# Optimization experiments

Measured on AMD Instinct MI355X. Metric: run time of the kernel, lower is better.

Reference implementation:

```python
import jax, jax.numpy as jnp
import numpy as np

B, T, E = 2, 4096, 768
H = 12
WIN = 256  # one-sided window w; band width = 2w+1


def setup_inputs() -> dict:
    key = jax.random.key(0)
    k1, k2, k3, k4 = jax.random.split(key, 4)
    scale = 1.0 / np.sqrt(E)
    return {
        "x": jax.random.normal(k1, (B, T, E), dtype=jnp.float32),
        "Wq": jax.random.normal(k2, (E, E), dtype=jnp.float32) * scale,
        "Wk": jax.random.normal(k3, (E, E), dtype=jnp.float32) * scale,
        "Wv": jax.random.normal(k4, (E, E), dtype=jnp.float32) * scale,
    }


def reference(x, Wq, Wk, Wv):
    b, t, e = x.shape
    h, w = H, WIN
    s = e // h
    Wb = 2 * w + 1          # band width
    nc = t // w             # number of query chunks of size w

    # projections (nn.Linear, bias=False): y = x @ W^T
    q = (x @ Wq.T).reshape(b, t, h, s) * (1.0 / np.sqrt(s))
    k = (x @ Wk.T).reshape(b, t, h, s)
    v = (x @ Wv.T).reshape(b, t, h, s)

    # overlapping key/value chunks: chunk c covers absolute keys [c*w - w, c*w + 2w)
    pad = [(0, 0), (w, w), (0, 0), (0, 0)]
    kp = jnp.pad(k, pad).reshape(b, nc + 2, w, h, s)
    k3 = jnp.concatenate([kp[:, :-2], kp[:, 1:-1], kp[:, 2:]], axis=2)  # [b,nc,3w,h,s]
    vp = jnp.pad(v, pad).reshape(b, nc + 2, w, h, s)
    v3 = jnp.concatenate([vp[:, :-2], vp[:, 1:-1], vp[:, 2:]], axis=2)  # [b,nc,3w,h,s]

    qc = q.reshape(b, nc, w, h, s)
    scores = jnp.einsum('bcxhd,bcyhd->bhcxy', qc, k3)  # [b,h,nc,w,3w]

    # extract the banded diagonals: band j <-> key index p + j in the 3w window
    idx = jnp.arange(w)[:, None] + jnp.arange(Wb)[None, :]  # [w, 2w+1], values in [0,3w)
    band = jnp.take_along_axis(scores, idx[None, None, None], axis=-1)  # [b,h,nc,w,2w+1]
    band = band.reshape(b, h, t, Wb).transpose(0, 2, 1, 3)  # [b,t,h,2w+1]

    # mask_invalid_locations: key absolute pos = i + j - w must lie in [0, t)
    key_pos = jnp.arange(t)[:, None] + jnp.arange(Wb)[None, :] - w
    invalid = (key_pos < 0) | (key_pos >= t)
    band = jnp.where(invalid[None, :, None, :], -jnp.inf, band)

    probs = jax.nn.softmax(band.astype(jnp.float32), axis=-1).astype(x.dtype)

    # sliding_chunks_matmul_pv: scatter band probs back to the 3w window layout
    pc = probs.transpose(0, 2, 1, 3).reshape(b, h, nc, w, Wb)
    pc_pad = jnp.pad(pc, [(0, 0)] * 4 + [(w - 1, w - 1)])  # last axis len 4w-1
    # full[p, m] = band[p, m - p] for m-p in [0, 2w], else 0
    idx2 = (jnp.arange(3 * w)[None, :] - jnp.arange(w)[:, None]) + (w - 1)  # [w, 3w]
    pfull = jnp.take_along_axis(pc_pad, idx2[None, None, None], axis=-1)  # [b,h,nc,w,3w]

    out = jnp.einsum('bhcpm,bcmhd->bcphd', pfull, v3).reshape(b, t, e)
    return out
```

## Files before the change

kernel.cpp:

```cpp
#include <hip/hip_runtime.h>

#define B_ 2
#define T_ 4096
#define E_ 768
#define H_ 12
#define S_ 64
#define WIN_ 256

typedef unsigned short u16;
typedef unsigned int u32;
typedef __attribute__((ext_vector_type(8))) short bf16x8;
typedef __attribute__((ext_vector_type(4))) short bf16x4;
typedef __attribute__((ext_vector_type(4))) float f32x4;

__device__ __forceinline__ u16 f2bf(float f) {
  u32 u = __float_as_uint(f);
  u += ((u >> 16) & 1u) + 0x7fffu;
  return (u16)(u >> 16);
}

__device__ __forceinline__ void async_copy16(const u16* g, u16* l) {
  __builtin_amdgcn_global_load_lds(
      (const __attribute__((address_space(1))) void*)g,
      (__attribute__((address_space(3))) void*)l, 16, 0, 0);
}

__global__ void cvt_all(const float* __restrict__ x, const float* __restrict__ wq,
                        const float* __restrict__ wk, const float* __restrict__ wv,
                        u16* __restrict__ xb, u16* __restrict__ wb) {
  const int n4x = B_ * T_ * E_ / 4;
  const int n4w = E_ * E_ / 4;
  int i = blockIdx.x * 256 + threadIdx.x;
  const float* src;
  u16* dst;
  int j;
  if (i < n4x) {
    src = x; dst = xb; j = i;
  } else {
    int t = i - n4x;
    int z = t / n4w;
    if (z >= 3) return;
    j = t - z * n4w;
    src = (z == 0) ? wq : ((z == 1) ? wk : wv);
    dst = wb + (size_t)z * E_ * E_;
  }
  float4 v = ((const float4*)src)[j];
  ushort4 o;
  o.x = f2bf(v.x); o.y = f2bf(v.y); o.z = f2bf(v.z); o.w = f2bf(v.w);
  ((ushort4*)dst)[j] = o;
}

__global__ __launch_bounds__(256)
void gemm_qkv(const u16* __restrict__ xb, const u16* __restrict__ wb,
              u16* __restrict__ qkv) {
  const int M = B_ * T_;
  __shared__ u16 As[3][128][32];
  __shared__ u16 Bs[3][128][32];
  int tid = threadIdx.x;
  int lane = tid & 63, wave = tid >> 6;
  int wr = wave >> 1, wc = wave & 1;
  int q8 = lane >> 4, nl = lane & 15;
  int bm = blockIdx.x * 128, bn = blockIdx.y * 128;
  int z = blockIdx.z;
  const u16* A = xb;
  const u16* Bmat = wb + (size_t)z * E_ * E_;
  u16* C = qkv + (size_t)z * M * E_;
  float scale = (z == 0) ? (0.125f * 1.44269504088896f) : 1.0f;

  int r0 = tid >> 2, c0 = tid & 3;
  int cs = c0 ^ (r0 & 3);
  const u16* ga0 = A + (size_t)(bm + r0) * E_ + cs * 8;
  const u16* ga1 = A + (size_t)(bm + r0 + 64) * E_ + cs * 8;
  const u16* gb0 = Bmat + (size_t)(bn + r0) * E_ + cs * 8;
  const u16* gb1 = Bmat + (size_t)(bn + r0 + 64) * E_ + cs * 8;
  int l0 = tid * 8;
  int l1 = tid * 8 + 2048;

  int swz8 = (q8 ^ (nl & 3)) * 8;

  const int NK = E_ / 32;
#pragma unroll
  for (int p = 0; p < 2; ++p) {
    int koff = p * 32;
    async_copy16(ga0 + koff, &As[p][0][0] + l0);
    async_copy16(ga1 + koff, &As[p][0][0] + l1);
    async_copy16(gb0 + koff, &Bs[p][0][0] + l0);
    async_copy16(gb1 + koff, &Bs[p][0][0] + l1);
  }

  f32x4 acc[4][4] = {};

#define KSTEP(KI, BUF, PBUF)                                                   \
  {                                                                            \
    asm volatile("s_waitcnt vmcnt(4) lgkmcnt(0)" ::: "memory");                \
    __builtin_amdgcn_s_barrier();                                              \
    __builtin_amdgcn_sched_barrier(0);                                         \
    int kp = ((KI) + 2 < NK) ? (KI) + 2 : NK - 1;                              \
    int koff = kp * 32;                                                        \
    async_copy16(ga0 + koff, &As[PBUF][0][0] + l0);                            \
    async_copy16(ga1 + koff, &As[PBUF][0][0] + l1);                            \
    async_copy16(gb0 + koff, &Bs[PBUF][0][0] + l0);                            \
    async_copy16(gb1 + koff, &Bs[PBUF][0][0] + l1);                            \
    bf16x8 af[4], bfr[4];                                                      \
    _Pragma("unroll")                                                          \
    for (int i = 0; i < 4; ++i)                                                \
      af[i] = *(const bf16x8*)&As[BUF][wr * 64 + i * 16 + nl][swz8];           \
    _Pragma("unroll")                                                          \
    for (int i = 0; i < 4; ++i)                                                \
      bfr[i] = *(const bf16x8*)&Bs[BUF][wc * 64 + i * 16 + nl][swz8];          \
    __builtin_amdgcn_s_setprio(1);                                             \
    _Pragma("unroll")                                                          \
    for (int i = 0; i < 4; ++i)                                                \
      _Pragma("unroll")                                                        \
      for (int j2 = 0; j2 < 4; ++j2)                                           \
        acc[i][j2] = __builtin_amdgcn_mfma_f32_16x16x32_bf16(af[i], bfr[j2],   \
                                                             acc[i][j2], 0, 0, 0); \
    __builtin_amdgcn_s_setprio(0);                                             \
  }

  for (int kb = 0; kb < NK; kb += 3) {
    KSTEP(kb + 0, 0, 2)
    KSTEP(kb + 1, 1, 0)
    KSTEP(kb + 2, 2, 1)
  }
#undef KSTEP

#pragma unroll
  for (int i = 0; i < 4; ++i)
#pragma unroll
    for (int j2 = 0; j2 < 4; ++j2)
#pragma unroll
      for (int r = 0; r < 4; ++r) {
        int row = bm + wr * 64 + i * 16 + q8 * 4 + r;
        int col = bn + wc * 64 + j2 * 16 + nl;
        C[(size_t)row * E_ + col] = f2bf(acc[i][j2][r] * scale);
      }
}

__global__ void transpose_v(const u16* __restrict__ v, u16* __restrict__ vT) {
  __shared__ u16 lt[64][66];
  int t = threadIdx.x;
  int t0 = blockIdx.x * 64;
  int e0 = blockIdx.y * 64;
  int b = blockIdx.z;
#pragma unroll
  for (int i = 0; i < 2; ++i) {
    int u = t + i * 256;
    int tok = u >> 3, cg = u & 7;
    bf16x8 val = *(const bf16x8*)(v + (size_t)(b * T_ + t0 + tok) * E_ + e0 + cg * 8);
#pragma unroll
    for (int j = 0; j < 8; ++j) lt[tok][cg * 8 + j] = (u16)val[j];
  }
  __syncthreads();
#pragma unroll
  for (int i = 0; i < 2; ++i) {
    int u = t + i * 256;
    int d = u >> 3, ck = u & 7;
    bf16x8 o;
#pragma unroll
    for (int j = 0; j < 8; ++j) o[j] = (short)lt[ck * 8 + j][d];
    *(bf16x8*)(vT + (size_t)(b * E_ + e0 + d) * T_ + t0 + ck * 8) = o;
  }
}

__global__ __launch_bounds__(256)
void attn_kernel(const u16* __restrict__ qkv, const u16* __restrict__ vT,
                 float* __restrict__ out) {
  const int Mtot = B_ * T_;
  const u16* qb = qkv;
  const u16* kb = qkv + (size_t)Mtot * E_;

  __shared__ u16 Pl[4][2][16][36];

  int tid = threadIdx.x;
  int lane = tid & 63, wave = tid >> 6;
  int q8 = lane >> 4, nl = lane & 15;
  int qs = blockIdx.x * 128;
  int bh = blockIdx.y;
  int b = bh / H_, h = bh % H_;
  int qw = qs + wave * 32;
  size_t ho = (size_t)h * S_;

  bf16x8 aq[2][2];
#pragma unroll
  for (int mt = 0; mt < 2; ++mt) {
    const u16* qrow = qb + (size_t)(b * T_ + qw + mt * 16 + nl) * E_ + ho;
    aq[mt][0] = *(const bf16x8*)(qrow + q8 * 8);
    aq[mt][1] = *(const bf16x8*)(qrow + 32 + q8 * 8);
  }

  f32x4 O[2][4] = {};
  f32x4 lacc[2] = {};

  int klo = qw - WIN_; if (klo < 0) klo = 0;
  int khi = qw + 32 + WIN_; if (khi > T_) khi = T_;

  const u16* kbase = kb + (size_t)b * T_ * E_ + ho;
  const u16* vbase = vT + (size_t)b * E_ * T_ + ho * T_;

  bf16x8 bk[2][2];
#pragma unroll
  for (int nt = 0; nt < 2; ++nt) {
    const u16* krow = kbase + (size_t)(klo + nt * 16 + nl) * E_;
    bk[nt][0] = *(const bf16x8*)(krow + q8 * 8);
    bk[nt][1] = *(const bf16x8*)(krow + 32 + q8 * 8);
  }

  for (int kt = klo; kt < khi; kt += 32) {
    bf16x8 bv[4];
#pragma unroll
    for (int dt = 0; dt < 4; ++dt)
      bv[dt] = *(const bf16x8*)(vbase + (size_t)(dt * 16 + nl) * T_ + kt + q8 * 8);

    int ktn = (kt + 32 < khi) ? kt + 32 : kt;
    bf16x8 nbk[2][2];
#pragma unroll
    for (int nt = 0; nt < 2; ++nt) {
      const u16* krow = kbase + (size_t)(ktn + nt * 16 + nl) * E_;
      nbk[nt][0] = *(const bf16x8*)(krow + q8 * 8);
      nbk[nt][1] = *(const bf16x8*)(krow + 32 + q8 * 8);
    }

    f32x4 sc[2][2] = {};
#pragma unroll
    for (int nt = 0; nt < 2; ++nt)
#pragma unroll
      for (int mt = 0; mt < 2; ++mt) {
        sc[mt][nt] = __builtin_amdgcn_mfma_f32_16x16x32_bf16(aq[mt][0], bk[nt][0], sc[mt][nt], 0, 0, 0);
        sc[mt][nt] = __builtin_amdgcn_mfma_f32_16x16x32_bf16(aq[mt][1], bk[nt][1], sc[mt][nt], 0, 0, 0);
      }

    if (kt < qw - 225 || kt > qw + 225) {
#pragma unroll
      for (int mt = 0; mt < 2; ++mt)
#pragma unroll
        for (int nt = 0; nt < 2; ++nt)
#pragma unroll
          for (int r = 0; r < 4; ++r) {
            int qa = qw + mt * 16 + q8 * 4 + r;
            int ka = kt + nt * 16 + nl;
            int d = ka - qa;
            sc[mt][nt][r] = (d < -WIN_ || d > WIN_) ? -1e30f : sc[mt][nt][r];
          }
    }

#pragma unroll
    for (int mt = 0; mt < 2; ++mt)
#pragma unroll
      for (int r = 0; r < 4; ++r) {
        float p0 = exp2f(sc[mt][0][r]);
        float p1 = exp2f(sc[mt][1][r]);
        sc[mt][0][r] = p0; sc[mt][1][r] = p1;
        lacc[mt][r] += p0 + p1;
      }

#pragma unroll
    for (int mt = 0; mt < 2; ++mt)
#pragma unroll
      for (int r = 0; r < 4; ++r) {
        Pl[wave][mt][q8 * 4 + r][nl] = f2bf(sc[mt][0][r]);
        Pl[wave][mt][q8 * 4 + r][16 + nl] = f2bf(sc[mt][1][r]);
      }

    bf16x8 ap[2];
#pragma unroll
    for (int mt = 0; mt < 2; ++mt) {
      bf16x4 lo = *(const bf16x4*)&Pl[wave][mt][nl][q8 * 8];
      bf16x4 hi = *(const bf16x4*)&Pl[wave][mt][nl][q8 * 8 + 4];
      bf16x8 a;
      a[0] = lo[0]; a[1] = lo[1]; a[2] = lo[2]; a[3] = lo[3];
      a[4] = hi[0]; a[5] = hi[1]; a[6] = hi[2]; a[7] = hi[3];
      ap[mt] = a;
    }

#pragma unroll
    for (int dt = 0; dt < 4; ++dt)
#pragma unroll
      for (int mt = 0; mt < 2; ++mt)
        O[mt][dt] = __builtin_amdgcn_mfma_f32_16x16x32_bf16(ap[mt], bv[dt], O[mt][dt], 0, 0, 0);

#pragma unroll
    for (int nt = 0; nt < 2; ++nt) {
      bk[nt][0] = nbk[nt][0];
      bk[nt][1] = nbk[nt][1];
    }
  }

#pragma unroll
  for (int mt = 0; mt < 2; ++mt)
#pragma unroll
    for (int r = 0; r < 4; ++r) {
      float l = lacc[mt][r];
      l += __shfl_xor(l, 1); l += __shfl_xor(l, 2);
      l += __shfl_xor(l, 4); l += __shfl_xor(l, 8);
      float inv = 1.0f / l;
      int qa = qw + mt * 16 + q8 * 4 + r;
      float* op = out + (size_t)(b * T_ + qa) * E_ + ho;
#pragma unroll
      for (int dt = 0; dt < 4; ++dt)
        op[dt * 16 + nl] = O[mt][dt][r] * inv;
    }
}

extern "C" void kernel_launch(void* const* d_in, const int* in_sizes, int n_in,
                              void* d_out, int out_size, void* d_ws, size_t ws_size,
                              hipStream_t stream) {
  const float* x  = (const float*)d_in[0];
  const float* Wq = (const float*)d_in[1];
  const float* Wk = (const float*)d_in[2];
  const float* Wv = (const float*)d_in[3];
  float* out = (float*)d_out;

  const size_t M = (size_t)B_ * T_;
  u16* xb  = (u16*)d_ws;
  u16* wb  = xb + M * E_;
  u16* qkv = wb + 3 * (size_t)E_ * E_;
  u16* vT  = xb;

  const int n4x = B_ * T_ * E_ / 4;
  const int n4w = E_ * E_ / 4;
  int cvt_blocks = (n4x + 3 * n4w + 255) / 256;
  cvt_all<<<cvt_blocks, 256, 0, stream>>>(x, Wq, Wk, Wv, xb, wb);

  dim3 g1(M / 128, E_ / 128, 3);
  gemm_qkv<<<g1, 256, 0, stream>>>(xb, wb, qkv);

  dim3 gt(T_ / 64, E_ / 64, B_);
  transpose_v<<<gt, 256, 0, stream>>>(qkv + 2 * M * E_, vT);

  dim3 g2(T_ / 128, B_ * H_);
  attn_kernel<<<g2, 256, 0, stream>>>(qkv, vT, out);
}
```

Before: 185.2 us.

## Split attention key range across wave pairs and combine partials via LDS

Each 32-query tile is now processed by two waves, each covering alternating 32-key tiles. The second wave writes its partial output and row sums to shared memory, and the first wave adds them before normalizing and storing. The grid doubles, which raises parallelism and shortens each wave's serial loop. In exchange it adds an LDS buffer, a block barrier and a reduction step, and relies on softmax needing no running max (the partials are simply summed).

```diff
diff --git a/kernel.cpp b/kernel.cpp
--- a/kernel.cpp
+++ b/kernel.cpp
@@ -171,14 +171,17 @@
   const u16* kb = qkv + (size_t)Mtot * E_;
 
   __shared__ u16 Pl[4][2][16][36];
+  __shared__ float cb[2][64][40];
 
   int tid = threadIdx.x;
   int lane = tid & 63, wave = tid >> 6;
+  int pair = wave >> 1;
+  int phase = wave & 1;
   int q8 = lane >> 4, nl = lane & 15;
-  int qs = blockIdx.x * 128;
+  int qs = blockIdx.x * 64;
   int bh = blockIdx.y;
   int b = bh / H_, h = bh % H_;
-  int qw = qs + wave * 32;
+  int qw = qs + pair * 32;
   size_t ho = (size_t)h * S_;
 
   bf16x8 aq[2][2];
@@ -194,6 +197,7 @@
 
   int klo = qw - WIN_; if (klo < 0) klo = 0;
   int khi = qw + 32 + WIN_; if (khi > T_) khi = T_;
+  int kst = klo + phase * 32;
 
   const u16* kbase = kb + (size_t)b * T_ * E_ + ho;
   const u16* vbase = vT + (size_t)b * E_ * T_ + ho * T_;
@@ -201,18 +205,18 @@
   bf16x8 bk[2][2];
 #pragma unroll
   for (int nt = 0; nt < 2; ++nt) {
-    const u16* krow = kbase + (size_t)(klo + nt * 16 + nl) * E_;
+    const u16* krow = kbase + (size_t)(kst + nt * 16 + nl) * E_;
     bk[nt][0] = *(const bf16x8*)(krow + q8 * 8);
     bk[nt][1] = *(const bf16x8*)(krow + 32 + q8 * 8);
   }
 
-  for (int kt = klo; kt < khi; kt += 32) {
+  for (int kt = kst; kt < khi; kt += 64) {
     bf16x8 bv[4];
 #pragma unroll
     for (int dt = 0; dt < 4; ++dt)
       bv[dt] = *(const bf16x8*)(vbase + (size_t)(dt * 16 + nl) * T_ + kt + q8 * 8);
 
-    int ktn = (kt + 32 < khi) ? kt + 32 : kt;
+    int ktn = (kt + 64 < khi) ? kt + 64 : kt;
     bf16x8 nbk[2][2];
 #pragma unroll
     for (int nt = 0; nt < 2; ++nt) {
@@ -286,20 +290,48 @@
     }
   }
 
-#pragma unroll
-  for (int mt = 0; mt < 2; ++mt)
-#pragma unroll
-    for (int r = 0; r < 4; ++r) {
-      float l = lacc[mt][r];
-      l += __shfl_xor(l, 1); l += __shfl_xor(l, 2);
-      l += __shfl_xor(l, 4); l += __shfl_xor(l, 8);
-      float inv = 1.0f / l;
-      int qa = qw + mt * 16 + q8 * 4 + r;
-      float* op = out + (size_t)(b * T_ + qa) * E_ + ho;
+  if (phase == 1) {
+    float* dst = &cb[pair][lane][0];
+#pragma unroll
+    for (int mt = 0; mt < 2; ++mt)
 #pragma unroll
       for (int dt = 0; dt < 4; ++dt)
-        op[dt * 16 + nl] = O[mt][dt][r] * inv;
-    }
+#pragma unroll
+        for (int r = 0; r < 4; ++r) dst[mt * 16 + dt * 4 + r] = O[mt][dt][r];
+#pragma unroll
+    for (int mt = 0; mt < 2; ++mt)
+#pragma unroll
+      for (int r = 0; r < 4; ++r) dst[32 + mt * 4 + r] = lacc[mt][r];
+  }
+  __syncthreads();
+  if (phase == 0) {
+    const float* src = &cb[pair][lane][0];
+#pragma unroll
+    for (int mt = 0; mt < 2; ++mt)
+#pragma unroll
+      for (int dt = 0; dt < 4; ++dt)
+#pragma unroll
+        for (int r = 0; r < 4; ++r) O[mt][dt][r] += src[mt * 16 + dt * 4 + r];
+#pragma unroll
+    for (int mt = 0; mt < 2; ++mt)
+#pragma unroll
+      for (int r = 0; r < 4; ++r) lacc[mt][r] += src[32 + mt * 4 + r];
+
+#pragma unroll
+    for (int mt = 0; mt < 2; ++mt)
+#pragma unroll
+      for (int r = 0; r < 4; ++r) {
+        float l = lacc[mt][r];
+        l += __shfl_xor(l, 1); l += __shfl_xor(l, 2);
+        l += __shfl_xor(l, 4); l += __shfl_xor(l, 8);
+        float inv = 1.0f / l;
+        int qa = qw + mt * 16 + q8 * 4 + r;
+        float* op = out + (size_t)(b * T_ + qa) * E_ + ho;
+#pragma unroll
+        for (int dt = 0; dt < 4; ++dt)
+          op[dt * 16 + nl] = O[mt][dt][r] * inv;
+      }
+  }
 }
 
 extern "C" void kernel_launch(void* const* d_in, const int* in_sizes, int n_in,
@@ -328,6 +360,6 @@
   dim3 gt(T_ / 64, E_ / 64, B_);
   transpose_v<<<gt, 256, 0, stream>>>(qkv + 2 * M * E_, vT);
 
-  dim3 g2(T_ / 128, B_ * H_);
+  dim3 g2(T_ / 64, B_ * H_);
   attn_kernel<<<g2, 256, 0, stream>>>(qkv, vT, out);
 }
```

After: 188.0 us. No clear change (+1.5%).

## Transpose score MFMA and redistribute P via ds_bpermute instead of LDS

Applied to the files above, without the earlier changes.

Swaps the MFMA operand order so each lane holds scores for one query row across keys, then packs probabilities to bf16 with v_cvt_pk_bf16_f32 and uses ds_bpermute to rearrange them into the A-operand layout for the PV MFMA. This removes the LDS round trip (store, reload) through the Pl buffer. The row-sum reduction changes to per-lane scalar sums followed by cross-quadrant shuffles. It also adds s_setprio around the MFMA blocks to favour matrix issue. The cost is extra bpermute and select instructions plus more complex lane mapping.

```diff
diff --git a/kernel.cpp b/kernel.cpp
--- a/kernel.cpp
+++ b/kernel.cpp
@@ -17,6 +17,12 @@
   u32 u = __float_as_uint(f);
   u += ((u >> 16) & 1u) + 0x7fffu;
   return (u16)(u >> 16);
+}
+
+__device__ __forceinline__ u32 cvt_pk_bf16(float lo, float hi) {
+  u32 r;
+  asm("v_cvt_pk_bf16_f32 %0, %1, %2" : "=v"(r) : "v"(lo), "v"(hi));
+  return r;
 }
 
 __device__ __forceinline__ void async_copy16(const u16* g, u16* l) {
@@ -170,8 +176,6 @@
   const u16* qb = qkv;
   const u16* kb = qkv + (size_t)Mtot * E_;
 
-  __shared__ u16 Pl[4][2][16][36];
-
   int tid = threadIdx.x;
   int lane = tid & 63, wave = tid >> 6;
   int q8 = lane >> 4, nl = lane & 15;
@@ -190,13 +194,17 @@
   }
 
   f32x4 O[2][4] = {};
-  f32x4 lacc[2] = {};
+  float lacc[2] = {0.f, 0.f};
 
   int klo = qw - WIN_; if (klo < 0) klo = 0;
   int khi = qw + 32 + WIN_; if (khi > T_) khi = T_;
 
   const u16* kbase = kb + (size_t)b * T_ * E_ + ho;
   const u16* vbase = vT + (size_t)b * E_ * T_ + ho * T_;
+
+  int alo = ((((q8 << 1) & 3) << 4) + nl) << 2;
+  int ahi = alo + 64;
+  bool hint = q8 >= 2;
 
   bf16x8 bk[2][2];
 #pragma unroll
@@ -222,13 +230,15 @@
     }
 
     f32x4 sc[2][2] = {};
+    __builtin_amdgcn_s_setprio(1);
 #pragma unroll
     for (int nt = 0; nt < 2; ++nt)
 #pragma unroll
       for (int mt = 0; mt < 2; ++mt) {
-        sc[mt][nt] = __builtin_amdgcn_mfma_f32_16x16x32_bf16(aq[mt][0], bk[nt][0], sc[mt][nt], 0, 0, 0);
-        sc[mt][nt] = __builtin_amdgcn_mfma_f32_16x16x32_bf16(aq[mt][1], bk[nt][1], sc[mt][nt], 0, 0, 0);
+        sc[mt][nt] = __builtin_amdgcn_mfma_f32_16x16x32_bf16(bk[nt][0], aq[mt][0], sc[mt][nt], 0, 0, 0);
+        sc[mt][nt] = __builtin_amdgcn_mfma_f32_16x16x32_bf16(bk[nt][1], aq[mt][1], sc[mt][nt], 0, 0, 0);
       }
+    __builtin_amdgcn_s_setprio(0);
 
     if (kt < qw - 225 || kt > qw + 225) {
 #pragma unroll
@@ -237,47 +247,57 @@
         for (int nt = 0; nt < 2; ++nt)
 #pragma unroll
           for (int r = 0; r < 4; ++r) {
-            int qa = qw + mt * 16 + q8 * 4 + r;
-            int ka = kt + nt * 16 + nl;
+            int qa = qw + mt * 16 + nl;
+            int ka = kt + nt * 16 + q8 * 4 + r;
             int d = ka - qa;
             sc[mt][nt][r] = (d < -WIN_ || d > WIN_) ? -1e30f : sc[mt][nt][r];
           }
     }
 
 #pragma unroll
-    for (int mt = 0; mt < 2; ++mt)
-#pragma unroll
-      for (int r = 0; r < 4; ++r) {
-        float p0 = exp2f(sc[mt][0][r]);
-        float p1 = exp2f(sc[mt][1][r]);
-        sc[mt][0][r] = p0; sc[mt][1][r] = p1;
-        lacc[mt][r] += p0 + p1;
-      }
-
-#pragma unroll
-    for (int mt = 0; mt < 2; ++mt)
-#pragma unroll
-      for (int r = 0; r < 4; ++r) {
-        Pl[wave][mt][q8 * 4 + r][nl] = f2bf(sc[mt][0][r]);
-        Pl[wave][mt][q8 * 4 + r][16 + nl] = f2bf(sc[mt][1][r]);
-      }
+    for (int mt = 0; mt < 2; ++mt) {
+      float s = 0.f;
+#pragma unroll
+      for (int nt = 0; nt < 2; ++nt)
+#pragma unroll
+        for (int r = 0; r < 4; ++r) {
+          float p = exp2f(sc[mt][nt][r]);
+          sc[mt][nt][r] = p;
+          s += p;
+        }
+      lacc[mt] += s;
+    }
 
     bf16x8 ap[2];
 #pragma unroll
     for (int mt = 0; mt < 2; ++mt) {
-      bf16x4 lo = *(const bf16x4*)&Pl[wave][mt][nl][q8 * 8];
-      bf16x4 hi = *(const bf16x4*)&Pl[wave][mt][nl][q8 * 8 + 4];
-      bf16x8 a;
-      a[0] = lo[0]; a[1] = lo[1]; a[2] = lo[2]; a[3] = lo[3];
-      a[4] = hi[0]; a[5] = hi[1]; a[6] = hi[2]; a[7] = hi[3];
-      ap[mt] = a;
-    }
-
+      u32 pk00 = cvt_pk_bf16(sc[mt][0][0], sc[mt][0][1]);
+      u32 pk01 = cvt_pk_bf16(sc[mt][0][2], sc[mt][0][3]);
+      u32 pk10 = cvt_pk_bf16(sc[mt][1][0], sc[mt][1][1]);
+      u32 pk11 = cvt_pk_bf16(sc[mt][1][2], sc[mt][1][3]);
+      int q0a = __builtin_amdgcn_ds_bpermute(alo, (int)pk00);
+      int q0b = __builtin_amdgcn_ds_bpermute(alo, (int)pk10);
+      int q1a = __builtin_amdgcn_ds_bpermute(alo, (int)pk01);
+      int q1b = __builtin_amdgcn_ds_bpermute(alo, (int)pk11);
+      int q2a = __builtin_amdgcn_ds_bpermute(ahi, (int)pk00);
+      int q2b = __builtin_amdgcn_ds_bpermute(ahi, (int)pk10);
+      int q3a = __builtin_amdgcn_ds_bpermute(ahi, (int)pk01);
+      int q3b = __builtin_amdgcn_ds_bpermute(ahi, (int)pk11);
+      union { u32 w[4]; bf16x8 v; } u;
+      u.w[0] = (u32)(hint ? q0b : q0a);
+      u.w[1] = (u32)(hint ? q1b : q1a);
+      u.w[2] = (u32)(hint ? q2b : q2a);
+      u.w[3] = (u32)(hint ? q3b : q3a);
+      ap[mt] = u.v;
+    }
+
+    __builtin_amdgcn_s_setprio(1);
 #pragma unroll
     for (int dt = 0; dt < 4; ++dt)
 #pragma unroll
       for (int mt = 0; mt < 2; ++mt)
         O[mt][dt] = __builtin_amdgcn_mfma_f32_16x16x32_bf16(ap[mt], bv[dt], O[mt][dt], 0, 0, 0);
+    __builtin_amdgcn_s_setprio(0);
 
 #pragma unroll
     for (int nt = 0; nt < 2; ++nt) {
@@ -287,13 +307,17 @@
   }
 
 #pragma unroll
+  for (int mt = 0; mt < 2; ++mt) {
+    lacc[mt] += __shfl_xor(lacc[mt], 16);
+    lacc[mt] += __shfl_xor(lacc[mt], 32);
+  }
+
+#pragma unroll
   for (int mt = 0; mt < 2; ++mt)
 #pragma unroll
     for (int r = 0; r < 4; ++r) {
-      float l = lacc[mt][r];
-      l += __shfl_xor(l, 1); l += __shfl_xor(l, 2);
-      l += __shfl_xor(l, 4); l += __shfl_xor(l, 8);
-      float inv = 1.0f / l;
+      float lq = __shfl(lacc[mt], (lane & 48) | (q8 * 4 + r));
+      float inv = 1.0f / lq;
       int qa = qw + mt * 16 + q8 * 4 + r;
       float* op = out + (size_t)(b * T_ + qa) * E_ + ho;
 #pragma unroll
```

After: 185.6 us. No clear change (+0.2%).
